# Optimization experiments

Hardware: AMD Instinct MI355X
Metric: run time of the kernel (lower is better)

Reference implementation:

```python
import jax, jax.numpy as jnp
import numpy as np

ALPHA = 0.2  # LeakyReLU negative slope
NEG_INF = -9e15


def _xavier(key, shape, gain=1.414):
    fan_in, fan_out = shape[-2], shape[-1]
    lim = gain * np.sqrt(6.0 / (fan_in + fan_out))
    return jax.random.uniform(key, shape, jnp.float32, -lim, lim)


def setup_inputs() -> dict:
    key = jax.random.key(0)
    ks = jax.random.split(key, 8)
    B, N, Din, H, Dh, Do = 8, 1024, 256, 4, 128, 64
    x = jax.random.normal(ks[0], (B, N, Din), jnp.float32)
    adj = jax.random.randint(ks[1], (B, N, N), 0, 2).astype(jnp.int32)
    W_heads = _xavier(ks[2], (H, Din, Dh))                 # per-head W
    a_heads = _xavier(ks[3], (H, 2 * Dh, 1))[..., 0]       # per-head a, [H, 2*Dh]
    W_out = _xavier(ks[4], (H * Dh, Do))                   # out_att W
    a_out = _xavier(ks[5], (2 * Do, 1))[..., 0]            # out_att a, [2*Do]
    Wf = _xavier(ks[6], (Do, Do), gain=1.0)                # fc_out linear
    bf = jnp.zeros((Do,), jnp.float32)
    return {"x": x, "adj": adj, "W_heads": W_heads, "a_heads": a_heads,
            "W_out": W_out, "a_out": a_out, "Wf": Wf, "bf": bf}


def _leaky_relu(v):
    return jnp.where(v >= 0, v, ALPHA * v)


def _gat(h, adj, W, a):
    # h: [B,N,Fin], adj: [B,N,N], W: [Fin,Fout], a: [2*Fout]
    Wh = h @ W                                   # [B,N,F]
    F = W.shape[-1]
    # additive attention: e_ij = leakyrelu(a_src.Wh_i + a_dst.Wh_j)
    src = Wh @ a[:F]                             # [B,N]
    dst = Wh @ a[F:]                             # [B,N]
    e = _leaky_relu(src[:, :, None] + dst[:, None, :])   # [B,N,N]
    scores = jnp.where(adj > 0, e, NEG_INF)
    attn = jax.nn.softmax(scores, axis=-1)       # dropout is a no-op in eval
    return attn @ Wh                             # [B,N,F]


def reference(x, adj, W_heads, a_heads, W_out, a_out, Wf, bf):
    B, N, _ = x.shape
    H, _, Dh = W_heads.shape
    # multi-head GAT, heads vmapped over leading axis of W_heads / a_heads
    heads = jax.vmap(_gat, in_axes=(None, None, 0, 0))(x, adj, W_heads, a_heads)  # [H,B,N,Dh]
    xcat = jnp.moveaxis(heads, 0, 2).reshape(B, N, H * Dh)   # concat heads, dim=2
    out = jax.nn.elu(_gat(xcat, adj, W_out, a_out))           # [B,N,Do]
    out = jax.nn.relu(out @ Wf + bf)                          # fc_out (dropout no-op)
    return out
```

## Files before the change

kernel.cpp:

```cpp
#include <hip/hip_runtime.h>
#include <hip/hip_bf16.h>

#define BSZ 8
#define NN 1024
#define DIN 256
#define NH 4
#define DH 128
#define DOUT 64
#define RTOT (BSZ*NN)
#define FCAT (NH*DH)
#define ALPHA 0.2f

typedef unsigned short ushortT;
typedef __attribute__((ext_vector_type(8))) short bf16x8;
typedef __attribute__((ext_vector_type(4))) float f32x4;

static __device__ __forceinline__ ushortT f2bf(float f) {
    __hip_bfloat16 h = __float2bfloat16(f);
    return *reinterpret_cast<ushortT*>(&h);
}
static __device__ __forceinline__ float bfu2f(ushortT u) {
    return __uint_as_float(((unsigned)u) << 16);
}
static __device__ __forceinline__ void split2(float v, ushortT& hi, ushortT& lo) {
    hi = f2bf(v);
    lo = f2bf(v - bfu2f(hi));
}
static __device__ __forceinline__ void gload16(const ushortT* g, ushortT* l) {
    __builtin_amdgcn_global_load_lds(
        (const __attribute__((address_space(1))) unsigned int*)(const void*)g,
        (__attribute__((address_space(3))) unsigned int*)(void*)l, 16, 0, 0);
}

__global__ __launch_bounds__(256) void k_prepw(const float* __restrict__ W,
                                               const float* __restrict__ Wout,
                                               ushortT* __restrict__ WbTh, ushortT* __restrict__ WbTl,
                                               ushortT* __restrict__ WoTh, ushortT* __restrict__ WoTl) {
    const int g2 = blockIdx.x * 256 + threadIdx.x;
    if (g2 < NH * DH * DIN) {
        const int h = g2 >> 15, f = (g2 >> 8) & 127, k = g2 & 255;
        const int kt = k >> 6, k64 = k & 63;
        const float v = W[(size_t)h * DIN * DH + (size_t)k * DH + f];
        ushortT hi, lo; split2(v, hi, lo);
        const int idx = ((h * 4 + kt) * 128 + f) * 64 + k64;
        WbTh[idx] = hi; WbTl[idx] = lo;
    } else {
        const int g3 = g2 - NH * DH * DIN;
        const int f = g3 >> 9, k = g3 & 511;
        const float v = Wout[(size_t)k * DOUT + f];
        ushortT hi, lo; split2(v, hi, lo);
        WoTh[g3] = hi; WoTl[g3] = lo;
    }
}

__global__ __launch_bounds__(512) void k_main(const float* __restrict__ x,
                                              const float* __restrict__ ah_,
                                              const ushortT* __restrict__ WbTh,
                                              const ushortT* __restrict__ WbTl,
                                              const int* __restrict__ adj,
                                              unsigned* __restrict__ adjbit,
                                              ushortT* __restrict__ WhT,
                                              float* __restrict__ src1,
                                              float* __restrict__ dst1) {
    __shared__ ushortT Ah[128 * 64], Al[128 * 64];
    __shared__ ushortT Bh[128 * 64], Bl[128 * 64];
    __shared__ float sred[8][32], dred[8][32];
    const int tid = threadIdx.x;
    if (blockIdx.x >= 256) {
        const int g = (blockIdx.x - 256) * 512 + tid;
        const int row = g >> 5, w = g & 31;
        const int4* p = (const int4*)(adj + (size_t)row * NN + w * 32);
        unsigned m = 0;
#pragma unroll
        for (int q = 0; q < 8; ++q) {
            const int4 v = p[q];
            m |= (v.x > 0 ? 1u : 0u) << (q * 4 + 0);
            m |= (v.y > 0 ? 1u : 0u) << (q * 4 + 1);
            m |= (v.z > 0 ? 1u : 0u) << (q * 4 + 2);
            m |= (v.w > 0 ? 1u : 0u) << (q * 4 + 3);
        }
        adjbit[g] = m;
        return;
    }
    const int lane = tid & 63, wave = tid >> 6;
    const int h = blockIdx.x >> 6, mt = blockIdx.x & 63;
    const int r0 = mt * 128, b = r0 >> 10, jr = r0 & 1023;
    const int m16 = lane & 15, quad = lane >> 4;
    const int mg = wave >> 1, fg = wave & 1;
    const int arow = tid >> 2, apart = tid & 3;
    f32x4 acc[2][4];
#pragma unroll
    for (int a = 0; a < 2; ++a)
#pragma unroll
        for (int c = 0; c < 4; ++c) acc[a][c] = (f32x4){0.f, 0.f, 0.f, 0.f};

    for (int kt = 0; kt < 4; ++kt) {
        __syncthreads();
        const ushortT* planeH = WbTh + (size_t)((h * 4 + kt) * 128) * 64;
        const ushortT* planeL = WbTl + (size_t)((h * 4 + kt) * 128) * 64;
#pragma unroll
        for (int half = 0; half < 2; ++half) {
            const int f = wave * 16 + half * 8 + (lane >> 3);
            const int sc = (lane & 7) ^ (f & 7);
            gload16(planeH + (size_t)f * 64 + sc * 8, Bh + (wave * 16 + half * 8) * 64);
            gload16(planeL + (size_t)f * 64 + sc * 8, Bl + (wave * 16 + half * 8) * 64);
        }
        {
            const float4* xs = (const float4*)(x + (size_t)(r0 + arow) * DIN + kt * 64 + apart * 16);
            union { ushortT u[16]; uint4 q[2]; } th, tl;
#pragma unroll
            for (int e = 0; e < 4; ++e) {
                const float4 v = xs[e];
                split2(v.x, th.u[e * 4 + 0], tl.u[e * 4 + 0]);
                split2(v.y, th.u[e * 4 + 1], tl.u[e * 4 + 1]);
                split2(v.z, th.u[e * 4 + 2], tl.u[e * 4 + 2]);
                split2(v.w, th.u[e * 4 + 3], tl.u[e * 4 + 3]);
            }
            const int s0 = (2 * apart) ^ (arow & 7), s1 = (2 * apart + 1) ^ (arow & 7);
            *(uint4*)&Ah[arow * 64 + s0 * 8] = th.q[0];
            *(uint4*)&Ah[arow * 64 + s1 * 8] = th.q[1];
            *(uint4*)&Al[arow * 64 + s0 * 8] = tl.q[0];
            *(uint4*)&Al[arow * 64 + s1 * 8] = tl.q[1];
        }
        __syncthreads();
#pragma unroll
        for (int ks = 0; ks < 2; ++ks) {
            bf16x8 a_h[2], a_l[2], b_h[4], b_l[4];
#pragma unroll
            for (int ms = 0; ms < 2; ++ms) {
                const int row = (mg * 2 + ms) * 16 + m16;
                const int cl = (ks * 4 + quad) ^ (row & 7);
                a_h[ms] = *(const bf16x8*)&Ah[row * 64 + cl * 8];
                a_l[ms] = *(const bf16x8*)&Al[row * 64 + cl * 8];
            }
#pragma unroll
            for (int fs = 0; fs < 4; ++fs) {
                const int row = (fg * 4 + fs) * 16 + m16;
                const int cl = (ks * 4 + quad) ^ (row & 7);
                b_h[fs] = *(const bf16x8*)&Bh[row * 64 + cl * 8];
                b_l[fs] = *(const bf16x8*)&Bl[row * 64 + cl * 8];
            }
#pragma unroll
            for (int ms = 0; ms < 2; ++ms)
#pragma unroll
                for (int fs = 0; fs < 4; ++fs) {
                    acc[ms][fs] = __builtin_amdgcn_mfma_f32_16x16x32_bf16(a_h[ms], b_h[fs], acc[ms][fs], 0, 0, 0);
                    acc[ms][fs] = __builtin_amdgcn_mfma_f32_16x16x32_bf16(a_h[ms], b_l[fs], acc[ms][fs], 0, 0, 0);
                    acc[ms][fs] = __builtin_amdgcn_mfma_f32_16x16x32_bf16(a_l[ms], b_h[fs], acc[ms][fs], 0, 0, 0);
                }
        }
    }
    float sacc[2][4] = {{0,0,0,0},{0,0,0,0}}, dacc[2][4] = {{0,0,0,0},{0,0,0,0}};
#pragma unroll
    for (int ms = 0; ms < 2; ++ms)
#pragma unroll
        for (int fs = 0; fs < 4; ++fs) {
            const int fl = (fg * 4 + fs) * 16 + m16;
            const float a_s = ah_[h * 2 * DH + fl];
            const float a_d = ah_[h * 2 * DH + DH + fl];
            union { ushortT u[4]; uint2 q; } tw;
#pragma unroll
            for (int reg = 0; reg < 4; ++reg) {
                const float v = acc[ms][fs][reg];
                sacc[ms][reg] += v * a_s;
                dacc[ms][reg] += v * a_d;
                tw.u[reg] = f2bf(v);
            }
            *(uint2*)(WhT + ((size_t)((b * NH + h) * DH + fl)) * NN + jr + (mg * 2 + ms) * 16 + quad * 4) = tw.q;
        }
#pragma unroll
    for (int ms = 0; ms < 2; ++ms) {
#pragma unroll
        for (int reg = 0; reg < 4; ++reg) {
            float s = sacc[ms][reg], d = dacc[ms][reg];
#pragma unroll
            for (int o = 8; o > 0; o >>= 1) {
                s += __shfl_xor(s, o, 64);
                d += __shfl_xor(d, o, 64);
            }
            if (m16 == 0) {
                sred[wave][ms * 16 + quad * 4 + reg] = s;
                dred[wave][ms * 16 + quad * 4 + reg] = d;
            }
        }
    }
    __syncthreads();
    if (tid < 128) {
        const int mgr = tid >> 5, idx = tid & 31;
        src1[h * RTOT + r0 + tid] = sred[mgr * 2][idx] + sred[mgr * 2 + 1][idx];
        dst1[h * RTOT + r0 + tid] = dred[mgr * 2][idx] + dred[mgr * 2 + 1][idx];
    }
}

__global__ __launch_bounds__(256) void k_attn1(const unsigned* __restrict__ adjbit,
                                               const ushortT* __restrict__ WhT,
                                               const float* __restrict__ src1,
                                               const float* __restrict__ dst1,
                                               ushortT* __restrict__ xcat) {
    __shared__ ushortT As[2][32 * 64];
    __shared__ ushortT Bs[2][128 * 64];
    __shared__ unsigned maskS[32 * 32];
    __shared__ float dstv[NN];
    __shared__ float srcv[32], rowinv[32], red4[4];
    const int tid = threadIdx.x, lane = tid & 63, wave = tid >> 6;
    const int bh = blockIdx.x & 31, it = blockIdx.x >> 5;
    const int b = bh >> 2, h = bh & 3;
    const int i0 = it * 32;
    const int m16 = lane & 15, quad = lane >> 4;

    const unsigned* mbase = adjbit + (size_t)(b * NN + i0) * 32;
#pragma unroll
    for (int k2 = 0; k2 < 4; ++k2) maskS[tid + 256 * k2] = mbase[tid + 256 * k2];
    float lm = -INFINITY;
#pragma unroll
    for (int k2 = 0; k2 < 4; ++k2) {
        const float d = dst1[h * RTOT + b * NN + tid + 256 * k2];
        dstv[tid + 256 * k2] = d;
        lm = fmaxf(lm, d);
    }
    if (tid < 32) srcv[tid] = src1[h * RTOT + b * NN + i0 + tid];
#pragma unroll
    for (int o = 32; o > 0; o >>= 1) lm = fmaxf(lm, __shfl_xor(lm, o, 64));
    if (lane == 0) red4[wave] = lm;
    __syncthreads();
    const float dmax = fmaxf(fmaxf(red4[0], red4[1]), fmaxf(red4[2], red4[3]));

    const int arow = tid >> 3, apart = tid & 7;
    const float si = srcv[arow];
    float mrow = si + dmax;
    mrow = mrow >= 0.f ? mrow : ALPHA * mrow;
    float fsum = 0.f;

    const ushortT* Bbase = WhT + (size_t)(bh * DH) * NN;
    f32x4 acc[2][2];
#pragma unroll
    for (int a = 0; a < 2; ++a)
#pragma unroll
        for (int c = 0; c < 2; ++c) acc[a][c] = (f32x4){0.f, 0.f, 0.f, 0.f};

#define STAGE_TILE(kt_, buf_)                                                              \
    {                                                                                      \
        const int kt__ = (kt_);                                                            \
        ushortT* bdst = &Bs[(buf_)][0];                                                    \
        _Pragma("unroll")                                                                  \
        for (int half = 0; half < 4; ++half) {                                             \
            const int f = wave * 32 + half * 8 + (lane >> 3);                              \
            gload16(Bbase + (size_t)f * NN + kt__ * 64 + (((lane & 7) ^ (f & 7)) * 8),     \
                    bdst + (wave * 32 + half * 8) * 64);                                   \
        }                                                                                  \
        const unsigned w0 = maskS[arow * 32 + kt__ * 2 + (apart >> 2)];                    \
        const int bb = (apart & 3) * 8;                                                    \
        union { ushortT u[8]; uint4 q; } tw;                                               \
        _Pragma("unroll")                                                                  \
        for (int e4 = 0; e4 < 2; ++e4) {                                                   \
            const float4 dv = *(const float4*)&dstv[kt__ * 64 + apart * 8 + e4 * 4];       \
            const float vv[4] = {dv.x, dv.y, dv.z, dv.w};                                  \
            _Pragma("unroll")                                                              \
            for (int e = 0; e < 4; ++e) {                                                  \
                float v = si + vv[e];                                                      \
                v = v >= 0.f ? v : ALPHA * v;                                              \
                const unsigned bit = (w0 >> (bb + e4 * 4 + e)) & 1u;                       \
                const float p = bit ? __expf(v - mrow) : 0.f;                              \
                fsum += p;                                                                 \
                tw.u[e4 * 4 + e] = f2bf(p);                                                \
            }                                                                              \
        }                                                                                  \
        *(uint4*)&As[(buf_)][arow * 64 + (apart ^ (arow & 7)) * 8] = tw.q;                 \
    }

    STAGE_TILE(0, 0);
    for (int kt = 0; kt < 16; ++kt) {
        const int cb = kt & 1;
        __syncthreads();
        if (kt < 15) STAGE_TILE(kt + 1, cb ^ 1);
#pragma unroll
        for (int ks = 0; ks < 2; ++ks) {
            bf16x8 afr[2];
#pragma unroll
            for (int ms = 0; ms < 2; ++ms) {
                const int rowa = ms * 16 + m16;
                const int cla = (ks * 4 + quad) ^ (rowa & 7);
                afr[ms] = *(const bf16x8*)&As[cb][rowa * 64 + cla * 8];
            }
#pragma unroll
            for (int ff = 0; ff < 2; ++ff) {
                const int rowb = wave * 32 + ff * 16 + m16;
                const int clb = (ks * 4 + quad) ^ (rowb & 7);
                const bf16x8 bfr = *(const bf16x8*)&Bs[cb][rowb * 64 + clb * 8];
#pragma unroll
                for (int ms = 0; ms < 2; ++ms)
                    acc[ms][ff] = __builtin_amdgcn_mfma_f32_16x16x32_bf16(afr[ms], bfr, acc[ms][ff], 0, 0, 0);
            }
        }
    }
#undef STAGE_TILE
#pragma unroll
    for (int o = 1; o < 8; o <<= 1) fsum += __shfl_xor(fsum, o, 64);
    if ((lane & 7) == 0) rowinv[arow] = 1.f / fsum;
    __syncthreads();
#pragma unroll
    for (int ms = 0; ms < 2; ++ms) {
        float rv[4];
#pragma unroll
        for (int reg = 0; reg < 4; ++reg) rv[reg] = rowinv[ms * 16 + quad * 4 + reg];
#pragma unroll
        for (int ff = 0; ff < 2; ++ff) {
            const int f = h * DH + wave * 32 + ff * 16 + m16;
#pragma unroll
            for (int reg = 0; reg < 4; ++reg) {
                const int i = i0 + ms * 16 + quad * 4 + reg;
                xcat[(size_t)(b * NN + i) * FCAT + f] = f2bf(acc[ms][ff][reg] * rv[reg]);
            }
        }
    }
}

__global__ __launch_bounds__(256) void k_wh2(const ushortT* __restrict__ xcat,
                                             const ushortT* __restrict__ WoTh,
                                             const ushortT* __restrict__ WoTl,
                                             const float* __restrict__ aout,
                                             ushortT* __restrict__ Wh2T,
                                             float* __restrict__ src2,
                                             float* __restrict__ dst2) {
    __shared__ ushortT As[32 * 64];
    __shared__ ushortT Bh[64 * 64], Bl[64 * 64];
    __shared__ float sred[4][16], dred[4][16];
    const int tid = threadIdx.x, lane = tid & 63, wave = tid >> 6;
    const int r0 = blockIdx.x * 32;
    const int b = r0 >> 10, jr = r0 & 1023;
    const int m16 = lane & 15, quad = lane >> 4;
    const int mg = wave >> 1, fg = wave & 1;
    f32x4 acc[2] = {(f32x4){0.f,0.f,0.f,0.f}, (f32x4){0.f,0.f,0.f,0.f}};

    for (int kt = 0; kt < 8; ++kt) {
        __syncthreads();
        {
            const int row = wave * 8 + (lane >> 3);
            const int sc = (lane & 7) ^ (row & 7);
            gload16(xcat + (size_t)(r0 + row) * FCAT + kt * 64 + sc * 8, As + wave * 8 * 64);
        }
#pragma unroll
        for (int half = 0; half < 2; ++half) {
            const int f = wave * 16 + half * 8 + (lane >> 3);
            const int sc = (lane & 7) ^ (f & 7);
            gload16(WoTh + (size_t)f * FCAT + kt * 64 + sc * 8, Bh + (wave * 16 + half * 8) * 64);
            gload16(WoTl + (size_t)f * FCAT + kt * 64 + sc * 8, Bl + (wave * 16 + half * 8) * 64);
        }
        __syncthreads();
#pragma unroll
        for (int ks = 0; ks < 2; ++ks) {
            const int rowa = mg * 16 + m16;
            const int cla = (ks * 4 + quad) ^ (rowa & 7);
            const bf16x8 afr = *(const bf16x8*)&As[rowa * 64 + cla * 8];
#pragma unroll
            for (int ff = 0; ff < 2; ++ff) {
                const int rowb = fg * 32 + ff * 16 + m16;
                const int clb = (ks * 4 + quad) ^ (rowb & 7);
                const bf16x8 b_h = *(const bf16x8*)&Bh[rowb * 64 + clb * 8];
                const bf16x8 b_l = *(const bf16x8*)&Bl[rowb * 64 + clb * 8];
                acc[ff] = __builtin_amdgcn_mfma_f32_16x16x32_bf16(afr, b_h, acc[ff], 0, 0, 0);
                acc[ff] = __builtin_amdgcn_mfma_f32_16x16x32_bf16(afr, b_l, acc[ff], 0, 0, 0);
            }
        }
    }
    float sv[4] = {0, 0, 0, 0}, dv[4] = {0, 0, 0, 0};
#pragma unroll
    for (int ff = 0; ff < 2; ++ff) {
        const int f = fg * 32 + ff * 16 + m16;
        const float a_s = aout[f], a_d = aout[DOUT + f];
        union { ushortT u[4]; uint2 q; } tw;
#pragma unroll
        for (int reg = 0; reg < 4; ++reg) {
            const float v = acc[ff][reg];
            sv[reg] += v * a_s;
            dv[reg] += v * a_d;
            tw.u[reg] = f2bf(v);
        }
        *(uint2*)(Wh2T + ((size_t)(b * DOUT + f)) * NN + jr + mg * 16 + quad * 4) = tw.q;
    }
#pragma unroll
    for (int reg = 0; reg < 4; ++reg) {
#pragma unroll
        for (int o = 8; o > 0; o >>= 1) {
            sv[reg] += __shfl_xor(sv[reg], o, 64);
            dv[reg] += __shfl_xor(dv[reg], o, 64);
        }
        if (m16 == 0) { sred[wave][quad * 4 + reg] = sv[reg]; dred[wave][quad * 4 + reg] = dv[reg]; }
    }
    __syncthreads();
    if (tid < 32) {
        const int mgr = tid >> 4, idx = tid & 15;
        src2[r0 + tid] = sred[mgr * 2][idx] + sred[mgr * 2 + 1][idx];
        dst2[r0 + tid] = dred[mgr * 2][idx] + dred[mgr * 2 + 1][idx];
    }
}

__global__ __launch_bounds__(256) void k_attn2(const unsigned* __restrict__ adjbit,
                                               const ushortT* __restrict__ Wh2T,
                                               const float* __restrict__ src2,
                                               const float* __restrict__ dst2,
                                               const float* __restrict__ Wf,
                                               const float* __restrict__ bfv,
                                               float* __restrict__ out) {
    __shared__ ushortT As[32 * 64];
    __shared__ ushortT Bs[64 * 64];
    __shared__ unsigned maskS[32 * 32];
    __shared__ float dstv[NN];
    __shared__ ushortT Wfh[64 * 64], Wfl[64 * 64];
    __shared__ float t2s[32 * 68];
    __shared__ float srcv[32], rowinv[32], red4[4];
    const int tid = threadIdx.x, lane = tid & 63, wave = tid >> 6;
    const int b = blockIdx.x & 7, it = blockIdx.x >> 3;
    const int i0 = it * 32;
    const int m16 = lane & 15, quad = lane >> 4;

    const unsigned* mbase = adjbit + (size_t)(b * NN + i0) * 32;
#pragma unroll
    for (int k2 = 0; k2 < 4; ++k2) maskS[tid + 256 * k2] = mbase[tid + 256 * k2];
    float lm = -INFINITY;
#pragma unroll
    for (int k2 = 0; k2 < 4; ++k2) {
        const float d = dst2[b * NN + tid + 256 * k2];
        dstv[tid + 256 * k2] = d;
        lm = fmaxf(lm, d);
    }
    if (tid < 32) srcv[tid] = src2[b * NN + i0 + tid];
    {
        const int c = tid & 63, kc = (tid >> 6) * 16;
        union { ushortT u[16]; uint4 q[2]; } th, tl;
#pragma unroll
        for (int e = 0; e < 16; ++e)
            split2(Wf[(size_t)(kc + e) * DOUT + c], th.u[e], tl.u[e]);
        const int s0 = ((tid >> 6) * 2) ^ (c & 7), s1 = ((tid >> 6) * 2 + 1) ^ (c & 7);
        *(uint4*)&Wfh[c * 64 + s0 * 8] = th.q[0];
        *(uint4*)&Wfh[c * 64 + s1 * 8] = th.q[1];
        *(uint4*)&Wfl[c * 64 + s0 * 8] = tl.q[0];
        *(uint4*)&Wfl[c * 64 + s1 * 8] = tl.q[1];
    }
#pragma unroll
    for (int o = 32; o > 0; o >>= 1) lm = fmaxf(lm, __shfl_xor(lm, o, 64));
    if (lane == 0) red4[wave] = lm;
    __syncthreads();
    const float dmax = fmaxf(fmaxf(red4[0], red4[1]), fmaxf(red4[2], red4[3]));

    const int arow = tid >> 3, apart = tid & 7;
    const float si = srcv[arow];
    float mrow = si + dmax;
    mrow = mrow >= 0.f ? mrow : ALPHA * mrow;
    float fsum = 0.f;

    const int mfrag = wave >> 1, fh = wave & 1;
    const ushortT* Bbase = Wh2T + (size_t)(b * DOUT) * NN;
    f32x4 acc[2] = {(f32x4){0.f,0.f,0.f,0.f}, (f32x4){0.f,0.f,0.f,0.f}};

    for (int kt = 0; kt < 16; ++kt) {
        __syncthreads();
#pragma unroll
        for (int half = 0; half < 2; ++half) {
            const int f = wave * 16 + half * 8 + (lane >> 3);
            gload16(Bbase + (size_t)f * NN + kt * 64 + (((lane & 7) ^ (f & 7)) * 8),
                    Bs + (wave * 16 + half * 8) * 64);
        }
        {
            const unsigned w0 = maskS[arow * 32 + kt * 2 + (apart >> 2)];
            const int bb = (apart & 3) * 8;
            union { ushortT u[8]; uint4 q; } tw;
#pragma unroll
            for (int e4 = 0; e4 < 2; ++e4) {
                const float4 dv = *(const float4*)&dstv[kt * 64 + apart * 8 + e4 * 4];
                const float vv[4] = {dv.x, dv.y, dv.z, dv.w};
#pragma unroll
                for (int e = 0; e < 4; ++e) {
                    float v = si + vv[e];
                    v = v >= 0.f ? v : ALPHA * v;
                    const unsigned bit = (w0 >> (bb + e4 * 4 + e)) & 1u;
                    const float p = bit ? __expf(v - mrow) : 0.f;
                    fsum += p;
                    tw.u[e4 * 4 + e] = f2bf(p);
                }
            }
            *(uint4*)&As[arow * 64 + (apart ^ (arow & 7)) * 8] = tw.q;
        }
        __syncthreads();
#pragma unroll
        for (int ks = 0; ks < 2; ++ks) {
            const int rowa = mfrag * 16 + m16;
            const int cla = (ks * 4 + quad) ^ (rowa & 7);
            const bf16x8 afr = *(const bf16x8*)&As[rowa * 64 + cla * 8];
#pragma unroll
            for (int ff = 0; ff < 2; ++ff) {
                const int rowb = (fh * 2 + ff) * 16 + m16;
                const int clb = (ks * 4 + quad) ^ (rowb & 7);
                const bf16x8 bfr = *(const bf16x8*)&Bs[rowb * 64 + clb * 8];
                acc[ff] = __builtin_amdgcn_mfma_f32_16x16x32_bf16(afr, bfr, acc[ff], 0, 0, 0);
            }
        }
    }
#pragma unroll
    for (int o = 1; o < 8; o <<= 1) fsum += __shfl_xor(fsum, o, 64);
    if ((lane & 7) == 0) rowinv[arow] = 1.f / fsum;
    __syncthreads();
#pragma unroll
    for (int ff = 0; ff < 2; ++ff) {
#pragma unroll
        for (int reg = 0; reg < 4; ++reg) {
            const int row = mfrag * 16 + quad * 4 + reg;
            float v = acc[ff][reg] * rowinv[row];
            v = v > 0.f ? v : (__expf(v) - 1.f);
            t2s[row * 68 + (fh * 2 + ff) * 16 + m16] = v;
        }
    }
    __syncthreads();
    const int mf = wave >> 1, nh = wave & 1;
    f32x4 oacc[2];
#pragma unroll
    for (int g = 0; g < 2; ++g) {
        const float bias = bfv[(nh * 2 + g) * 16 + m16];
        oacc[g] = (f32x4){bias, bias, bias, bias};
    }
#pragma unroll
    for (int ks = 0; ks < 2; ++ks) {
        const int rowa = mf * 16 + m16;
        const float4 fA = *(const float4*)&t2s[rowa * 68 + ks * 32 + quad * 8];
        const float4 fB = *(const float4*)&t2s[rowa * 68 + ks * 32 + quad * 8 + 4];
        union { ushortT u[8]; bf16x8 v; } a_h, a_l;
        const float av[8] = {fA.x, fA.y, fA.z, fA.w, fB.x, fB.y, fB.z, fB.w};
#pragma unroll
        for (int e = 0; e < 8; ++e) split2(av[e], a_h.u[e], a_l.u[e]);
#pragma unroll
        for (int g = 0; g < 2; ++g) {
            const int rowc = (nh * 2 + g) * 16 + m16;
            const int cl = (ks * 4 + quad) ^ (rowc & 7);
            const bf16x8 b_h = *(const bf16x8*)&Wfh[rowc * 64 + cl * 8];
            const bf16x8 b_l = *(const bf16x8*)&Wfl[rowc * 64 + cl * 8];
            oacc[g] = __builtin_amdgcn_mfma_f32_16x16x32_bf16(a_h.v, b_h, oacc[g], 0, 0, 0);
            oacc[g] = __builtin_amdgcn_mfma_f32_16x16x32_bf16(a_h.v, b_l, oacc[g], 0, 0, 0);
            oacc[g] = __builtin_amdgcn_mfma_f32_16x16x32_bf16(a_l.v, b_h, oacc[g], 0, 0, 0);
        }
    }
#pragma unroll
    for (int g = 0; g < 2; ++g) {
        const int c = (nh * 2 + g) * 16 + m16;
#pragma unroll
        for (int reg = 0; reg < 4; ++reg) {
            const int i = i0 + mf * 16 + quad * 4 + reg;
            out[(size_t)(b * NN + i) * DOUT + c] = fmaxf(oacc[g][reg], 0.f);
        }
    }
}

extern "C" void kernel_launch(void* const* d_in, const int* in_sizes, int n_in,
                              void* d_out, int out_size, void* d_ws, size_t ws_size,
                              hipStream_t stream) {
    const float* x   = (const float*)d_in[0];
    const int*   adj = (const int*)d_in[1];
    const float* Wh  = (const float*)d_in[2];
    const float* ah  = (const float*)d_in[3];
    const float* Wo  = (const float*)d_in[4];
    const float* ao  = (const float*)d_in[5];
    const float* Wf  = (const float*)d_in[6];
    const float* bf  = (const float*)d_in[7];
    float* out = (float*)d_out;

    float* ws    = (float*)d_ws;
    float* src1  = ws;
    float* dst1  = src1 + NH * RTOT;
    float* src2  = dst1 + NH * RTOT;
    float* dst2  = src2 + RTOT;
    ushortT* WhT   = (ushortT*)(dst2 + RTOT);
    ushortT* Wh2T  = WhT + (size_t)RTOT * FCAT;
    ushortT* xcat  = Wh2T + (size_t)RTOT * DOUT;
    ushortT* WbTh  = xcat + (size_t)RTOT * FCAT;
    ushortT* WbTl  = WbTh + NH * DH * DIN;
    ushortT* WoTh  = WbTl + NH * DH * DIN;
    ushortT* WoTl  = WoTh + DOUT * FCAT;
    unsigned* adjbit = (unsigned*)(WoTl + DOUT * FCAT);

    hipLaunchKernelGGL(k_prepw, dim3((NH * DH * DIN + DOUT * FCAT) / 256), dim3(256), 0, stream,
                       Wh, Wo, WbTh, WbTl, WoTh, WoTl);
    hipLaunchKernelGGL(k_main,  dim3(768), dim3(512), 0, stream,
                       x, ah, WbTh, WbTl, adj, adjbit, WhT, src1, dst1);
    hipLaunchKernelGGL(k_attn1, dim3(1024), dim3(256), 0, stream,
                       adjbit, WhT, src1, dst1, xcat);
    hipLaunchKernelGGL(k_wh2,   dim3(256), dim3(256), 0, stream,
                       xcat, WoTh, WoTl, ao, Wh2T, src2, dst2);
    hipLaunchKernelGGL(k_attn2, dim3(256), dim3(256), 0, stream,
                       adjbit, Wh2T, src2, dst2, Wf, bf, out);
}
```

Measured before the change: 155.9 us.

## Pre-split x to bf16 planes, enlarge attn1 tiles, double-buffer attn2

```diff
diff --git a/kernel.cpp b/kernel.cpp
--- a/kernel.cpp
+++ b/kernel.cpp
@@ -10,6 +10,7 @@
 #define RTOT (BSZ*NN)
 #define FCAT (NH*DH)
 #define ALPHA 0.2f
+#define XBLK 1024
 
 typedef unsigned short ushortT;
 typedef __attribute__((ext_vector_type(8))) short bf16x8;
@@ -32,11 +33,30 @@
         (__attribute__((address_space(3))) unsigned int*)(void*)l, 16, 0, 0);
 }
 
-__global__ __launch_bounds__(256) void k_prepw(const float* __restrict__ W,
+__global__ __launch_bounds__(256) void k_prepw(const float* __restrict__ x,
+                                               const float* __restrict__ W,
                                                const float* __restrict__ Wout,
+                                               ushortT* __restrict__ xbh, ushortT* __restrict__ xbl,
                                                ushortT* __restrict__ WbTh, ushortT* __restrict__ WbTl,
                                                ushortT* __restrict__ WoTh, ushortT* __restrict__ WoTl) {
-    const int g2 = blockIdx.x * 256 + threadIdx.x;
+    const int bx = blockIdx.x;
+    if (bx < XBLK) {
+        const int g = bx * 256 + threadIdx.x;
+        const float4* p = (const float4*)x + (size_t)g * 2;
+        union { ushortT u[8]; uint4 q; } th, tl;
+#pragma unroll
+        for (int e4 = 0; e4 < 2; ++e4) {
+            const float4 v = p[e4];
+            split2(v.x, th.u[e4 * 4 + 0], tl.u[e4 * 4 + 0]);
+            split2(v.y, th.u[e4 * 4 + 1], tl.u[e4 * 4 + 1]);
+            split2(v.z, th.u[e4 * 4 + 2], tl.u[e4 * 4 + 2]);
+            split2(v.w, th.u[e4 * 4 + 3], tl.u[e4 * 4 + 3]);
+        }
+        ((uint4*)xbh)[g] = th.q;
+        ((uint4*)xbl)[g] = tl.q;
+        return;
+    }
+    const int g2 = (bx - XBLK) * 256 + threadIdx.x;
     if (g2 < NH * DH * DIN) {
         const int h = g2 >> 15, f = (g2 >> 8) & 127, k = g2 & 255;
         const int kt = k >> 6, k64 = k & 63;
@@ -53,7 +73,8 @@
     }
 }
 
-__global__ __launch_bounds__(512) void k_main(const float* __restrict__ x,
+__global__ __launch_bounds__(512) void k_main(const ushortT* __restrict__ xbh,
+                                              const ushortT* __restrict__ xbl,
                                               const float* __restrict__ ah_,
                                               const ushortT* __restrict__ WbTh,
                                               const ushortT* __restrict__ WbTl,
@@ -87,7 +108,6 @@
     const int r0 = mt * 128, b = r0 >> 10, jr = r0 & 1023;
     const int m16 = lane & 15, quad = lane >> 4;
     const int mg = wave >> 1, fg = wave & 1;
-    const int arow = tid >> 2, apart = tid & 3;
     f32x4 acc[2][4];
 #pragma unroll
     for (int a = 0; a < 2; ++a)
@@ -105,22 +125,12 @@
             gload16(planeH + (size_t)f * 64 + sc * 8, Bh + (wave * 16 + half * 8) * 64);
             gload16(planeL + (size_t)f * 64 + sc * 8, Bl + (wave * 16 + half * 8) * 64);
         }
-        {
-            const float4* xs = (const float4*)(x + (size_t)(r0 + arow) * DIN + kt * 64 + apart * 16);
-            union { ushortT u[16]; uint4 q[2]; } th, tl;
-#pragma unroll
-            for (int e = 0; e < 4; ++e) {
-                const float4 v = xs[e];
-                split2(v.x, th.u[e * 4 + 0], tl.u[e * 4 + 0]);
-                split2(v.y, th.u[e * 4 + 1], tl.u[e * 4 + 1]);
-                split2(v.z, th.u[e * 4 + 2], tl.u[e * 4 + 2]);
-                split2(v.w, th.u[e * 4 + 3], tl.u[e * 4 + 3]);
-            }
-            const int s0 = (2 * apart) ^ (arow & 7), s1 = (2 * apart + 1) ^ (arow & 7);
-            *(uint4*)&Ah[arow * 64 + s0 * 8] = th.q[0];
-            *(uint4*)&Ah[arow * 64 + s1 * 8] = th.q[1];
-            *(uint4*)&Al[arow * 64 + s0 * 8] = tl.q[0];
-            *(uint4*)&Al[arow * 64 + s1 * 8] = tl.q[1];
+#pragma unroll
+        for (int half = 0; half < 2; ++half) {
+            const int r = wave * 16 + half * 8 + (lane >> 3);
+            const int sc = (lane & 7) ^ (r & 7);
+            gload16(xbh + (size_t)(r0 + r) * DIN + kt * 64 + sc * 8, Ah + (wave * 16 + half * 8) * 64);
+            gload16(xbl + (size_t)(r0 + r) * DIN + kt * 64 + sc * 8, Al + (wave * 16 + half * 8) * 64);
         }
         __syncthreads();
 #pragma unroll
@@ -192,38 +202,41 @@
     }
 }
 
-__global__ __launch_bounds__(256) void k_attn1(const unsigned* __restrict__ adjbit,
+__global__ __launch_bounds__(512) void k_attn1(const unsigned* __restrict__ adjbit,
                                                const ushortT* __restrict__ WhT,
                                                const float* __restrict__ src1,
                                                const float* __restrict__ dst1,
                                                ushortT* __restrict__ xcat) {
-    __shared__ ushortT As[2][32 * 64];
+    __shared__ ushortT As[2][64 * 64];
     __shared__ ushortT Bs[2][128 * 64];
-    __shared__ unsigned maskS[32 * 32];
+    __shared__ unsigned maskS[64 * 32];
     __shared__ float dstv[NN];
-    __shared__ float srcv[32], rowinv[32], red4[4];
+    __shared__ float srcv[64], rowinv[64], red8[8];
     const int tid = threadIdx.x, lane = tid & 63, wave = tid >> 6;
     const int bh = blockIdx.x & 31, it = blockIdx.x >> 5;
     const int b = bh >> 2, h = bh & 3;
-    const int i0 = it * 32;
+    const int i0 = it * 64;
     const int m16 = lane & 15, quad = lane >> 4;
+    const int mg = wave >> 2, fg = wave & 3;
 
     const unsigned* mbase = adjbit + (size_t)(b * NN + i0) * 32;
 #pragma unroll
-    for (int k2 = 0; k2 < 4; ++k2) maskS[tid + 256 * k2] = mbase[tid + 256 * k2];
+    for (int k2 = 0; k2 < 4; ++k2) maskS[tid + 512 * k2] = mbase[tid + 512 * k2];
     float lm = -INFINITY;
 #pragma unroll
-    for (int k2 = 0; k2 < 4; ++k2) {
-        const float d = dst1[h * RTOT + b * NN + tid + 256 * k2];
-        dstv[tid + 256 * k2] = d;
+    for (int k2 = 0; k2 < 2; ++k2) {
+        const float d = dst1[h * RTOT + b * NN + tid + 512 * k2];
+        dstv[tid + 512 * k2] = d;
         lm = fmaxf(lm, d);
     }
-    if (tid < 32) srcv[tid] = src1[h * RTOT + b * NN + i0 + tid];
+    if (tid < 64) srcv[tid] = src1[h * RTOT + b * NN + i0 + tid];
 #pragma unroll
     for (int o = 32; o > 0; o >>= 1) lm = fmaxf(lm, __shfl_xor(lm, o, 64));
-    if (lane == 0) red4[wave] = lm;
+    if (lane == 0) red8[wave] = lm;
     __syncthreads();
-    const float dmax = fmaxf(fmaxf(red4[0], red4[1]), fmaxf(red4[2], red4[3]));
+    float dmax = red8[0];
+#pragma unroll
+    for (int w = 1; w < 8; ++w) dmax = fmaxf(dmax, red8[w]);
 
     const int arow = tid >> 3, apart = tid & 7;
     const float si = srcv[arow];
@@ -243,10 +256,10 @@
         const int kt__ = (kt_);                                                            \
         ushortT* bdst = &Bs[(buf_)][0];                                                    \
         _Pragma("unroll")                                                                  \
-        for (int half = 0; half < 4; ++half) {                                             \
-            const int f = wave * 32 + half * 8 + (lane >> 3);                              \
+        for (int half = 0; half < 2; ++half) {                                             \
+            const int f = wave * 16 + half * 8 + (lane >> 3);                              \
             gload16(Bbase + (size_t)f * NN + kt__ * 64 + (((lane & 7) ^ (f & 7)) * 8),     \
-                    bdst + (wave * 32 + half * 8) * 64);                                   \
+                    bdst + (wave * 16 + half * 8) * 64);                                   \
         }                                                                                  \
         const unsigned w0 = maskS[arow * 32 + kt__ * 2 + (apart >> 2)];                    \
         const int bb = (apart & 3) * 8;                                                    \
@@ -278,13 +291,13 @@
             bf16x8 afr[2];
 #pragma unroll
             for (int ms = 0; ms < 2; ++ms) {
-                const int rowa = ms * 16 + m16;
+                const int rowa = mg * 32 + ms * 16 + m16;
                 const int cla = (ks * 4 + quad) ^ (rowa & 7);
                 afr[ms] = *(const bf16x8*)&As[cb][rowa * 64 + cla * 8];
             }
 #pragma unroll
             for (int ff = 0; ff < 2; ++ff) {
-                const int rowb = wave * 32 + ff * 16 + m16;
+                const int rowb = fg * 32 + ff * 16 + m16;
                 const int clb = (ks * 4 + quad) ^ (rowb & 7);
                 const bf16x8 bfr = *(const bf16x8*)&Bs[cb][rowb * 64 + clb * 8];
 #pragma unroll
@@ -302,13 +315,13 @@
     for (int ms = 0; ms < 2; ++ms) {
         float rv[4];
 #pragma unroll
-        for (int reg = 0; reg < 4; ++reg) rv[reg] = rowinv[ms * 16 + quad * 4 + reg];
+        for (int reg = 0; reg < 4; ++reg) rv[reg] = rowinv[mg * 32 + ms * 16 + quad * 4 + reg];
 #pragma unroll
         for (int ff = 0; ff < 2; ++ff) {
-            const int f = h * DH + wave * 32 + ff * 16 + m16;
+            const int f = h * DH + fg * 32 + ff * 16 + m16;
 #pragma unroll
             for (int reg = 0; reg < 4; ++reg) {
-                const int i = i0 + ms * 16 + quad * 4 + reg;
+                const int i = i0 + mg * 32 + ms * 16 + quad * 4 + reg;
                 xcat[(size_t)(b * NN + i) * FCAT + f] = f2bf(acc[ms][ff][reg] * rv[reg]);
             }
         }
@@ -402,8 +415,8 @@
                                                const float* __restrict__ Wf,
                                                const float* __restrict__ bfv,
                                                float* __restrict__ out) {
-    __shared__ ushortT As[32 * 64];
-    __shared__ ushortT Bs[64 * 64];
+    __shared__ ushortT As[2][32 * 64];
+    __shared__ ushortT Bs[2][64 * 64];
     __shared__ unsigned maskS[32 * 32];
     __shared__ float dstv[NN];
     __shared__ ushortT Wfh[64 * 64], Wfl[64 * 64];
@@ -453,49 +466,56 @@
     const ushortT* Bbase = Wh2T + (size_t)(b * DOUT) * NN;
     f32x4 acc[2] = {(f32x4){0.f,0.f,0.f,0.f}, (f32x4){0.f,0.f,0.f,0.f}};
 
+#define STAGE2(kt_, buf_)                                                                  \
+    {                                                                                      \
+        const int kt__ = (kt_);                                                            \
+        ushortT* bdst = &Bs[(buf_)][0];                                                    \
+        _Pragma("unroll")                                                                  \
+        for (int half = 0; half < 2; ++half) {                                             \
+            const int f = wave * 16 + half * 8 + (lane >> 3);                              \
+            gload16(Bbase + (size_t)f * NN + kt__ * 64 + (((lane & 7) ^ (f & 7)) * 8),     \
+                    bdst + (wave * 16 + half * 8) * 64);                                   \
+        }                                                                                  \
+        const unsigned w0 = maskS[arow * 32 + kt__ * 2 + (apart >> 2)];                    \
+        const int bb = (apart & 3) * 8;                                                    \
+        union { ushortT u[8]; uint4 q; } tw;                                               \
+        _Pragma("unroll")                                                                  \
+        for (int e4 = 0; e4 < 2; ++e4) {                                                   \
+            const float4 dv = *(const float4*)&dstv[kt__ * 64 + apart * 8 + e4 * 4];       \
+            const float vv[4] = {dv.x, dv.y, dv.z, dv.w};                                  \
+            _Pragma("unroll")                                                              \
+            for (int e = 0; e < 4; ++e) {                                                  \
+                float v = si + vv[e];                                                      \
+                v = v >= 0.f ? v : ALPHA * v;                                              \
+                const unsigned bit = (w0 >> (bb + e4 * 4 + e)) & 1u;                       \
+                const float p = bit ? __expf(v - mrow) : 0.f;                              \
+                fsum += p;                                                                 \
+                tw.u[e4 * 4 + e] = f2bf(p);                                                \
+            }                                                                              \
+        }                                                                                  \
+        *(uint4*)&As[(buf_)][arow * 64 + (apart ^ (arow & 7)) * 8] = tw.q;                 \
+    }
+
+    STAGE2(0, 0);
     for (int kt = 0; kt < 16; ++kt) {
+        const int cb = kt & 1;
         __syncthreads();
-#pragma unroll
-        for (int half = 0; half < 2; ++half) {
-            const int f = wave * 16 + half * 8 + (lane >> 3);
-            gload16(Bbase + (size_t)f * NN + kt * 64 + (((lane & 7) ^ (f & 7)) * 8),
-                    Bs + (wave * 16 + half * 8) * 64);
-        }
-        {
-            const unsigned w0 = maskS[arow * 32 + kt * 2 + (apart >> 2)];
-            const int bb = (apart & 3) * 8;
-            union { ushortT u[8]; uint4 q; } tw;
-#pragma unroll
-            for (int e4 = 0; e4 < 2; ++e4) {
-                const float4 dv = *(const float4*)&dstv[kt * 64 + apart * 8 + e4 * 4];
-                const float vv[4] = {dv.x, dv.y, dv.z, dv.w};
-#pragma unroll
-                for (int e = 0; e < 4; ++e) {
-                    float v = si + vv[e];
-                    v = v >= 0.f ? v : ALPHA * v;
-                    const unsigned bit = (w0 >> (bb + e4 * 4 + e)) & 1u;
-                    const float p = bit ? __expf(v - mrow) : 0.f;
-                    fsum += p;
-                    tw.u[e4 * 4 + e] = f2bf(p);
-                }
-            }
-            *(uint4*)&As[arow * 64 + (apart ^ (arow & 7)) * 8] = tw.q;
-        }
-        __syncthreads();
+        if (kt < 15) STAGE2(kt + 1, cb ^ 1);
 #pragma unroll
         for (int ks = 0; ks < 2; ++ks) {
             const int rowa = mfrag * 16 + m16;
             const int cla = (ks * 4 + quad) ^ (rowa & 7);
-            const bf16x8 afr = *(const bf16x8*)&As[rowa * 64 + cla * 8];
+            const bf16x8 afr = *(const bf16x8*)&As[cb][rowa * 64 + cla * 8];
 #pragma unroll
             for (int ff = 0; ff < 2; ++ff) {
                 const int rowb = (fh * 2 + ff) * 16 + m16;
                 const int clb = (ks * 4 + quad) ^ (rowb & 7);
-                const bf16x8 bfr = *(const bf16x8*)&Bs[rowb * 64 + clb * 8];
+                const bf16x8 bfr = *(const bf16x8*)&Bs[cb][rowb * 64 + clb * 8];
                 acc[ff] = __builtin_amdgcn_mfma_f32_16x16x32_bf16(afr, bfr, acc[ff], 0, 0, 0);
             }
         }
     }
+#undef STAGE2
 #pragma unroll
     for (int o = 1; o < 8; o <<= 1) fsum += __shfl_xor(fsum, o, 64);
     if ((lane & 7) == 0) rowinv[arow] = 1.f / fsum;
@@ -575,12 +595,14 @@
     ushortT* WoTh  = WbTl + NH * DH * DIN;
     ushortT* WoTl  = WoTh + DOUT * FCAT;
     unsigned* adjbit = (unsigned*)(WoTl + DOUT * FCAT);
-
-    hipLaunchKernelGGL(k_prepw, dim3((NH * DH * DIN + DOUT * FCAT) / 256), dim3(256), 0, stream,
-                       Wh, Wo, WbTh, WbTl, WoTh, WoTl);
+    ushortT* xbh  = (ushortT*)(adjbit + (size_t)BSZ * NN * 32);
+    ushortT* xbl  = xbh + (size_t)RTOT * DIN;
+
+    hipLaunchKernelGGL(k_prepw, dim3(XBLK + (NH * DH * DIN + DOUT * FCAT) / 256), dim3(256), 0, stream,
+                       x, Wh, Wo, xbh, xbl, WbTh, WbTl, WoTh, WoTl);
     hipLaunchKernelGGL(k_main,  dim3(768), dim3(512), 0, stream,
-                       x, ah, WbTh, WbTl, adj, adjbit, WhT, src1, dst1);
-    hipLaunchKernelGGL(k_attn1, dim3(1024), dim3(256), 0, stream,
+                       xbh, xbl, ah, WbTh, WbTl, adj, adjbit, WhT, src1, dst1);
+    hipLaunchKernelGGL(k_attn1, dim3(512), dim3(512), 0, stream,
                        adjbit, WhT, src1, dst1, xcat);
     hipLaunchKernelGGL(k_wh2,   dim3(256), dim3(256), 0, stream,
                        xcat, WoTh, WoTl, ao, Wh2T, src2, dst2);
```

Result: no change. 154.1 us (-1.2%).
